# Kernel optimization log

Hardware: AMD Instinct MI355X
Metric: run time of the kernel (lower is better)

Reference implementation:

```python
import jax, jax.numpy as jnp
import numpy as np

B, S, D, H = 2, 2048, 1024, 16
HD = D // H  # head_dim = 64


def setup_inputs() -> dict:
    key = jax.random.key(0)
    ks = jax.random.split(key, 7)
    scale = 0.02
    return {
        "q": jax.random.normal(ks[0], (B, S, D), dtype=jnp.float32),
        "k": jax.random.normal(ks[1], (B, S, D), dtype=jnp.float32),
        "v": jax.random.normal(ks[2], (B, S, D), dtype=jnp.float32),
        "Wq": jax.random.normal(ks[3], (D, D), dtype=jnp.float32) * scale,
        "Wk": jax.random.normal(ks[4], (D, D), dtype=jnp.float32) * scale,
        "Wv": jax.random.normal(ks[5], (D, D), dtype=jnp.float32) * scale,
        "Wo": jax.random.normal(ks[6], (D, D), dtype=jnp.float32) * scale,
    }


def reference(q, k, v, Wq, Wk, Wv, Wo):
    # bias-free linear projections (torch Linear: y = x @ W.T)
    qh = (q @ Wq.T).reshape(B, S, H, HD).transpose(0, 2, 1, 3)  # b h t d
    kh = (k @ Wk.T).reshape(B, S, H, HD).transpose(0, 2, 1, 3)
    vh = (v @ Wv.T).reshape(B, S, H, HD).transpose(0, 2, 1, 3)

    scores = jnp.einsum("bhqd,bhkd->bhqk", qh, kh) / jnp.sqrt(jnp.float32(HD))
    # max_subtract: NOTE faithful to source - max taken BEFORE causal masking
    scores = scores - jnp.max(scores, axis=-1, keepdims=True)
    # causal mask (strict upper triangle -> -inf)
    causal_mask = jnp.triu(jnp.ones((S, S), dtype=bool), k=1)
    scores = jnp.where(causal_mask, -jnp.inf, scores)
    num = jnp.exp(scores)
    den = jnp.sum(num, axis=-1, keepdims=True) + 1.0  # quiet softmax (+1 denominator)
    attn = num / den

    out = jnp.einsum("bhqk,bhkd->bhqd", attn, vh)
    out = out.transpose(0, 2, 1, 3).reshape(B, S, D)  # b t (h d)
    return out @ Wo.T
```

## Files before the change

kernel.cpp:

```cpp
#include <hip/hip_runtime.h>
#include <hip/hip_bf16.h>

#define B_  2
#define S_  2048
#define D_  1024
#define H_  16
#define HD_ 64

typedef __attribute__((ext_vector_type(4))) short s16x4;
typedef __attribute__((ext_vector_type(8))) short s16x8;
typedef __attribute__((ext_vector_type(4))) float f32x4;
typedef __attribute__((ext_vector_type(8))) __bf16 bf16x8;

__device__ __forceinline__ unsigned short f2bf(float x) {
  union { float f; unsigned int u; } un; un.f = x;
  unsigned int r = un.u + 0x7fffu + ((un.u >> 16) & 1u);
  return (unsigned short)(r >> 16);
}

__device__ __forceinline__ f32x4 fz4() { f32x4 z = {0.f, 0.f, 0.f, 0.f}; return z; }

__device__ __forceinline__ f32x4 mfma32(s16x8 a, s16x8 b, f32x4 c) {
  return __builtin_amdgcn_mfma_f32_16x16x32_bf16(
      __builtin_bit_cast(bf16x8, a), __builtin_bit_cast(bf16x8, b), c, 0, 0, 0);
}

__device__ __forceinline__ void gload16(void* lds_base, const void* gsrc) {
  __builtin_amdgcn_global_load_lds(
      (const __attribute__((address_space(1))) unsigned int*)gsrc,
      (__attribute__((address_space(3))) unsigned int*)lds_base, 16, 0, 0);
}

__global__ __launch_bounds__(256) void cvt_all(const float4* __restrict__ q,
                                               const float4* __restrict__ k,
                                               const float4* __restrict__ v,
                                               const float4* __restrict__ wq,
                                               const float4* __restrict__ wk,
                                               const float4* __restrict__ wv,
                                               const float4* __restrict__ wo,
                                               uint2* __restrict__ oq, uint2* __restrict__ ok,
                                               uint2* __restrict__ ov, uint2* __restrict__ owq,
                                               uint2* __restrict__ owk, uint2* __restrict__ owv,
                                               uint2* __restrict__ owo) {
  int i = blockIdx.x * 256 + threadIdx.x;
  int st = gridDim.x * 256;
  for (; i < 4194304; i += st) {
    const float4* s; uint2* d; int off;
    if (i < 3145728) {
      int t = i >> 20; off = i & 1048575;
      s = (t == 0) ? q : (t == 1 ? k : v);
      d = (t == 0) ? oq : (t == 1 ? ok : ov);
    } else {
      int j = i - 3145728;
      int t = j >> 18; off = j & 262143;
      s = (t == 0) ? wq : (t == 1 ? wk : (t == 2 ? wv : wo));
      d = (t == 0) ? owq : (t == 1 ? owk : (t == 2 ? owv : owo));
    }
    float4 x = s[off];
    uint2 o;
    o.x = (unsigned)f2bf(x.x) | ((unsigned)f2bf(x.y) << 16);
    o.y = (unsigned)f2bf(x.z) | ((unsigned)f2bf(x.w) << 16);
    d[off] = o;
  }
}

template<int BM, int MODE, int NG>
__global__ __launch_bounds__(256) void gemm_bt(
    const unsigned short* __restrict__ A0, const unsigned short* __restrict__ A1,
    const unsigned short* __restrict__ A2,
    const unsigned short* __restrict__ W0, const unsigned short* __restrict__ W1,
    const unsigned short* __restrict__ W2,
    unsigned short* __restrict__ ob0, unsigned short* __restrict__ ob1,
    unsigned short* __restrict__ ob2, float* __restrict__ of) {
  __shared__ unsigned short As[2][BM * 32];
  __shared__ unsigned short Bs[2][128 * 32];
  const int tid  = threadIdx.x;
  const int lane = tid & 63;
  const int w    = tid >> 6;
  const int l15  = lane & 15, g = lane >> 4;

  int m0, n0;
  const unsigned short *A, *W;
  unsigned short* obf;
  float scale = 1.0f;
  if (NG == 3) {
    int swz = ((int)blockIdx.x & 7) * 96 + ((int)blockIdx.x >> 3);
    int p  = swz >> 5;
    int gi = p >> 3;
    n0 = (p & 7) * 128;
    m0 = (swz & 31) * 128;
    A   = gi == 0 ? A0 : (gi == 1 ? A1 : A2);
    W   = gi == 0 ? W0 : (gi == 1 ? W1 : W2);
    obf = gi == 0 ? ob0 : (gi == 1 ? ob1 : ob2);
    scale = (gi == 0) ? 0.125f : 1.0f;
  } else {
    int swz = ((int)blockIdx.x & 7) * 64 + ((int)blockIdx.x >> 3);
    m0 = (swz & 63) * BM;
    n0 = (swz >> 6) * 128;
    A = A0; W = W0; obf = ob0;
  }

  constexpr int MI  = (BM == 128) ? 4 : 2;
  const int wr = (w >> 1) * (MI * 16);
  const int wc = (w & 1) * 64;

  f32x4 acc[MI][4];
  #pragma unroll
  for (int i = 0; i < MI; i++)
    #pragma unroll
    for (int j = 0; j < 4; j++) acc[i][j] = fz4();

  const int srow = w * 16 + (lane >> 2);
  const int scol = ((lane & 3) ^ ((lane >> 2) & 3)) * 8;

  #define STAGE(buf, k0)                                                          \
    {                                                                             \
      _Pragma("unroll")                                                           \
      for (int i = 0; i < BM / 64; i++)                                           \
        gload16(&As[buf][(i * 64 + w * 16) * 32],                                 \
                &A[(size_t)(m0 + i * 64 + srow) * D_ + (k0) + scol]);             \
      _Pragma("unroll")                                                           \
      for (int i = 0; i < 2; i++)                                                 \
        gload16(&Bs[buf][(i * 64 + w * 16) * 32],                                 \
                &W[(size_t)(n0 + i * 64 + srow) * D_ + (k0) + scol]);             \
    }

  STAGE(0, 0);
  __syncthreads();
  int buf = 0;
  for (int t = 0; t < 32; ++t) {
    if (t < 31) STAGE(buf ^ 1, (t + 1) * 32);
    s16x8 af[MI], bfr[4];
    #pragma unroll
    for (int mi = 0; mi < MI; mi++)
      af[mi] = *(const s16x8*)&As[buf][(wr + mi * 16 + l15) * 32 + ((g ^ (l15 & 3)) * 8)];
    #pragma unroll
    for (int ni = 0; ni < 4; ni++)
      bfr[ni] = *(const s16x8*)&Bs[buf][(wc + ni * 16 + l15) * 32 + ((g ^ (l15 & 3)) * 8)];
    __builtin_amdgcn_s_setprio(1);
    #pragma unroll
    for (int mi = 0; mi < MI; mi++)
      #pragma unroll
      for (int ni = 0; ni < 4; ni++)
        acc[mi][ni] = mfma32(af[mi], bfr[ni], acc[mi][ni]);
    __builtin_amdgcn_s_setprio(0);
    __syncthreads();
    buf ^= 1;
  }
  #undef STAGE

  #pragma unroll
  for (int mi = 0; mi < MI; mi++)
    #pragma unroll
    for (int ni = 0; ni < 4; ni++)
      #pragma unroll
      for (int j = 0; j < 4; j++) {
        int r = m0 + wr + mi * 16 + 4 * g + j;
        int c = n0 + wc + ni * 16 + l15;
        float v = acc[mi][ni][j] * scale;
        if (MODE == 0) {
          int b = r >> 11, s = r & (S_ - 1), h = c >> 6, hd = c & 63;
          obf[(((size_t)(b * H_ + h)) * S_ + s) * HD_ + hd] = f2bf(v);
        } else {
          of[(size_t)r * D_ + c] = v;
        }
      }
}

__global__ __launch_bounds__(512) void attn_kernel(const unsigned short* __restrict__ Qh,
                                                   const unsigned short* __restrict__ Kh,
                                                   const unsigned short* __restrict__ Vh,
                                                   unsigned short* __restrict__ AO) {
  __shared__ unsigned short Ks[2][64 * 64];
  __shared__ unsigned short Vt[2][64 * 76];
  const int tid  = threadIdx.x;
  const int lane = tid & 63;
  const int w    = tid >> 6;
  const int wq   = w & 3;
  const int grp  = w >> 2;
  const int l15  = lane & 15, g = lane >> 4;

  int swz = ((int)blockIdx.x & 7) * 64 + ((int)blockIdx.x >> 3);
  const int bh = swz >> 4;
  const int pr = swz & 15;
  const int qtA = pr, qtB = 31 - pr;
  const int myqt  = grp ? qtB : qtA;
  const int qtMax = qtB;
  const int q0 = myqt * 64;
  const unsigned short* Qb = Qh + (size_t)bh * S_ * HD_;
  const unsigned short* Kb = Kh + (size_t)bh * S_ * HD_;
  const unsigned short* Vb = Vh + (size_t)bh * S_ * HD_;

  const int qrow = q0 + wq * 16 + l15;
  s16x8 qf[2];
  #pragma unroll
  for (int kk = 0; kk < 2; kk++)
    qf[kk] = *(const s16x8*)&Qb[(size_t)qrow * HD_ + kk * 32 + 8 * g];

  float m = -INFINITY, l = 0.f;
  f32x4 outa[4];
  #pragma unroll
  for (int d = 0; d < 4; d++) outa[d] = fz4();

  const int srow_l = lane >> 3;
  const int scol = ((lane & 7) ^ ((lane >> 3) & 7)) * 8;
  const int vkey = tid & 63;
  const int vhd0 = (tid >> 6) * 8;

  #define STAGE_K(kblk, b)                                                        \
    gload16(&Ks[b][(w * 8) * 64],                                                 \
            &Kb[(size_t)((kblk) * 64 + w * 8 + srow_l) * HD_ + scol]);
  #define LOAD_V(kblk, vr)                                                        \
    vr = *(const uint4*)&Vb[(size_t)((kblk) * 64 + vkey) * HD_ + vhd0];
  #define WRITE_V(b, vr)                                                          \
    {                                                                             \
      unsigned int u[4] = {vr.x, vr.y, vr.z, vr.w};                               \
      _Pragma("unroll")                                                           \
      for (int c2 = 0; c2 < 4; c2++) {                                            \
        Vt[b][(vhd0 + 2 * c2    ) * 76 + vkey] = (unsigned short)(u[c2] & 0xffffu); \
        Vt[b][(vhd0 + 2 * c2 + 1) * 76 + vkey] = (unsigned short)(u[c2] >> 16);   \
      }                                                                           \
    }

  {
    STAGE_K(0, 0);
    uint4 vr0;
    LOAD_V(0, vr0);
    WRITE_V(0, vr0);
    __syncthreads();
  }

  for (int t = 0; t < 32; ++t) {
    const int cur = t & 1, nxt = cur ^ 1;
    const int k0 = t * 64;
    if (t < 31) STAGE_K(t + 1, nxt);
    uint4 vr;
    const bool vnext = (t < 31) && (t + 1 <= qtMax);
    if (vnext) LOAD_V(t + 1, vr);

    f32x4 sf[4];
    #pragma unroll
    for (int kt = 0; kt < 4; kt++) sf[kt] = fz4();
    __builtin_amdgcn_s_setprio(1);
    #pragma unroll
    for (int kt = 0; kt < 4; kt++)
      #pragma unroll
      for (int kk = 0; kk < 2; kk++) {
        s16x8 kf = *(const s16x8*)&Ks[cur][(kt * 16 + l15) * 64 + (((kk * 4 + g) ^ (l15 & 7)) * 8)];
        sf[kt] = mfma32(kf, qf[kk], sf[kt]);
      }
    __builtin_amdgcn_s_setprio(0);

    float bm = -INFINITY;
    #pragma unroll
    for (int kt = 0; kt < 4; kt++)
      #pragma unroll
      for (int j = 0; j < 4; j++) bm = fmaxf(bm, sf[kt][j]);
    bm = fmaxf(bm, __shfl_xor(bm, 16));
    bm = fmaxf(bm, __shfl_xor(bm, 32));
    if (__any(bm > m)) {
      float mn  = fmaxf(m, bm);
      float fsc = __expf(m - mn);
      m = mn;
      l *= fsc;
      #pragma unroll
      for (int d = 0; d < 4; d++)
        #pragma unroll
        for (int j = 0; j < 4; j++) outa[d][j] *= fsc;
    }

    if (t <= myqt) {
      s16x8 pfs[2];
      float rs = 0.f;
      if (t == myqt) {
        #pragma unroll
        for (int kt2 = 0; kt2 < 2; kt2++)
          #pragma unroll
          for (int j = 0; j < 4; j++) {
            int keyg = k0 + kt2 * 32 + 4 * g + j;
            float e = (keyg <= qrow) ? __expf(sf[2 * kt2][j] - m) : 0.f;
            rs += e;
            pfs[kt2][j] = (short)f2bf(e);
            float e2 = (keyg + 16 <= qrow) ? __expf(sf[2 * kt2 + 1][j] - m) : 0.f;
            rs += e2;
            pfs[kt2][4 + j] = (short)f2bf(e2);
          }
      } else {
        #pragma unroll
        for (int kt2 = 0; kt2 < 2; kt2++)
          #pragma unroll
          for (int j = 0; j < 4; j++) {
            float e = __expf(sf[2 * kt2][j] - m);
            rs += e;
            pfs[kt2][j] = (short)f2bf(e);
            float e2 = __expf(sf[2 * kt2 + 1][j] - m);
            rs += e2;
            pfs[kt2][4 + j] = (short)f2bf(e2);
          }
      }
      rs += __shfl_xor(rs, 16);
      rs += __shfl_xor(rs, 32);
      l += rs;
      __builtin_amdgcn_s_setprio(1);
      #pragma unroll
      for (int d = 0; d < 4; d++)
        #pragma unroll
        for (int kt2 = 0; kt2 < 2; kt2++) {
          s16x4 vlo = *(const s16x4*)&Vt[cur][(d * 16 + l15) * 76 + kt2 * 32 + 4 * g];
          s16x4 vhi = *(const s16x4*)&Vt[cur][(d * 16 + l15) * 76 + kt2 * 32 + 16 + 4 * g];
          s16x8 vv = {vlo[0], vlo[1], vlo[2], vlo[3], vhi[0], vhi[1], vhi[2], vhi[3]};
          outa[d] = mfma32(vv, pfs[kt2], outa[d]);
        }
      __builtin_amdgcn_s_setprio(0);
    }

    if (vnext) WRITE_V(nxt, vr);
    __syncthreads();
  }
  #undef STAGE_K
  #undef LOAD_V
  #undef WRITE_V

  const float inv = 1.f / (l + 1.f);
  const int b = bh >> 4, h = bh & 15;
  #pragma unroll
  for (int d = 0; d < 4; d++) {
    uint2 o;
    o.x = (unsigned)f2bf(outa[d][0] * inv) | ((unsigned)f2bf(outa[d][1] * inv) << 16);
    o.y = (unsigned)f2bf(outa[d][2] * inv) | ((unsigned)f2bf(outa[d][3] * inv) << 16);
    *(uint2*)&AO[(size_t)(b * S_ + qrow) * D_ + h * 64 + d * 16 + 4 * g] = o;
  }
}

extern "C" void kernel_launch(void* const* d_in, const int* in_sizes, int n_in,
                              void* d_out, int out_size, void* d_ws, size_t ws_size,
                              hipStream_t stream) {
  const float* q  = (const float*)d_in[0];
  const float* k  = (const float*)d_in[1];
  const float* v  = (const float*)d_in[2];
  const float* Wq = (const float*)d_in[3];
  const float* Wk = (const float*)d_in[4];
  const float* Wv = (const float*)d_in[5];
  const float* Wo = (const float*)d_in[6];

  unsigned short* ws  = (unsigned short*)d_ws;
  unsigned short* qb  = ws;
  unsigned short* kb  = qb  + 4194304;
  unsigned short* vb  = kb  + 4194304;
  unsigned short* Wqb = vb  + 4194304;
  unsigned short* Wkb = Wqb + 1048576;
  unsigned short* Wvb = Wkb + 1048576;
  unsigned short* Wob = Wvb + 1048576;
  unsigned short* Qh  = Wob + 1048576;
  unsigned short* Kh  = Qh  + 4194304;
  unsigned short* Vh  = Kh  + 4194304;
  unsigned short* AO  = Vh  + 4194304;

  cvt_all<<<2048, 256, 0, stream>>>((const float4*)q, (const float4*)k, (const float4*)v,
                                    (const float4*)Wq, (const float4*)Wk, (const float4*)Wv,
                                    (const float4*)Wo,
                                    (uint2*)qb, (uint2*)kb, (uint2*)vb, (uint2*)Wqb,
                                    (uint2*)Wkb, (uint2*)Wvb, (uint2*)Wob);

  gemm_bt<128, 0, 3><<<768, 256, 0, stream>>>(qb, kb, vb, Wqb, Wkb, Wvb,
                                              Qh, Kh, Vh, nullptr);

  attn_kernel<<<512, 512, 0, stream>>>(Qh, Kh, Vh, AO);

  gemm_bt<64, 1, 1><<<512, 256, 0, stream>>>(AO, nullptr, nullptr, Wob, nullptr, nullptr,
                                             nullptr, nullptr, nullptr, (float*)d_out);
}
```

Baseline: 223.9 us.

## Replace QKV projection GEMM with 256x256-tile, 8-wave pipelined kernel

The fused QKV projection moves from 128x128 tiles with 4 waves and BK=32 to 256x256 tiles with 8 waves and BK=64. Each 256-row A slice and W slice is then loaded far fewer times, cutting global and LDS traffic per MFMA. Global loads for the next K tile are interleaved with MFMA quadrants using explicit vmcnt/lgkmcnt waits and barriers, with XOR-swizzled LDS addressing. The cost is 192 blocks on a GPU with many CUs, which may underfill the device, plus heavy register pressure from 128 accumulator vectors per thread. The output projection is split into its own specialised kernel with no functional change.

```diff
diff --git a/kernel.cpp b/kernel.cpp
--- a/kernel.cpp
+++ b/kernel.cpp
@@ -64,49 +64,145 @@
   }
 }
 
-template<int BM, int MODE, int NG>
-__global__ __launch_bounds__(256) void gemm_bt(
+__global__ __launch_bounds__(512, 2) void qkv256(
     const unsigned short* __restrict__ A0, const unsigned short* __restrict__ A1,
     const unsigned short* __restrict__ A2,
     const unsigned short* __restrict__ W0, const unsigned short* __restrict__ W1,
     const unsigned short* __restrict__ W2,
     unsigned short* __restrict__ ob0, unsigned short* __restrict__ ob1,
-    unsigned short* __restrict__ ob2, float* __restrict__ of) {
-  __shared__ unsigned short As[2][BM * 32];
+    unsigned short* __restrict__ ob2) {
+  __shared__ unsigned short As[2][16384];
+  __shared__ unsigned short Bs[2][16384];
+  const int tid  = threadIdx.x;
+  const int lane = tid & 63;
+  const int w    = tid >> 6;
+  const int l15  = lane & 15, g = lane >> 4;
+  const int wm   = w >> 2;
+  const int wn   = w & 3;
+
+  int swz = ((int)blockIdx.x & 7) * 24 + ((int)blockIdx.x >> 3);
+  const int nt = swz / 48;
+  const int mt = swz % 48;
+  const int gi = mt >> 4;
+  const int m0 = (mt & 15) * 256;
+  const int n0 = nt * 256;
+  const unsigned short* A = gi == 0 ? A0 : (gi == 1 ? A1 : A2);
+  const unsigned short* W = gi == 0 ? W0 : (gi == 1 ? W1 : W2);
+  unsigned short* obf     = gi == 0 ? ob0 : (gi == 1 ? ob1 : ob2);
+  const float scale = (gi == 0) ? 0.125f : 1.0f;
+
+  f32x4 acc[8][4];
+  #pragma unroll
+  for (int i = 0; i < 8; i++)
+    #pragma unroll
+    for (int j = 0; j < 4; j++) acc[i][j] = fz4();
+
+  const int srow_i = w * 8 + (lane >> 3);
+  const int scol   = ((lane & 7) ^ ((lane >> 3) & 7)) * 8;
+
+  #define SG_A(nb, i, kt) gload16(&As[nb][((i) * 512 + w * 64) * 8],                     \
+      &A[(size_t)(m0 + (i) * 64 + srow_i) * D_ + (kt) * 64 + scol])
+  #define SG_B(nb, i, kt) gload16(&Bs[nb][((i) * 512 + w * 64) * 8],                     \
+      &W[(size_t)(n0 + (i) * 64 + srow_i) * D_ + (kt) * 64 + scol])
+
+  #define RD_A(dst, mq, bufi)                                                            \
+    _Pragma("unroll") for (int fi = 0; fi < 4; fi++)                                     \
+      _Pragma("unroll") for (int kk = 0; kk < 2; kk++)                                   \
+        dst[fi][kk] = *(const s16x8*)&As[bufi][(wm * 128 + (mq) * 64 + fi * 16 + l15) * 64 \
+                                              + (((kk * 4 + g) ^ (l15 & 7)) * 8)];
+  #define RD_B(dst, nq, bufi)                                                            \
+    _Pragma("unroll") for (int fj = 0; fj < 2; fj++)                                     \
+      _Pragma("unroll") for (int kk = 0; kk < 2; kk++)                                   \
+        dst[fj][kk] = *(const s16x8*)&Bs[bufi][(wn * 64 + (nq) * 32 + fj * 16 + l15) * 64  \
+                                              + (((kk * 4 + g) ^ (l15 & 7)) * 8)];
+  #define MM(mq, nq, av, bv)                                                             \
+    _Pragma("unroll") for (int fi = 0; fi < 4; fi++)                                     \
+      _Pragma("unroll") for (int fj = 0; fj < 2; fj++)                                   \
+        _Pragma("unroll") for (int kk = 0; kk < 2; kk++)                                 \
+          acc[(mq) * 4 + fi][(nq) * 2 + fj] =                                            \
+              mfma32(av[fi][kk], bv[fj][kk], acc[(mq) * 4 + fi][(nq) * 2 + fj]);
+
+  SG_A(0, 0, 0); SG_A(0, 2, 0);
+  SG_B(0, 0, 0); SG_B(0, 1, 0); SG_B(0, 2, 0); SG_B(0, 3, 0);
+  SG_A(0, 1, 0); SG_A(0, 3, 0);
+
+  s16x8 a[4][2], b0[2][2], b1[2][2];
+  for (int t = 0; t < 16; ++t) {
+    const int buf = t & 1, nb = buf ^ 1;
+    const int tn = (t + 1) & 15;
+    asm volatile("s_waitcnt vmcnt(2)" ::: "memory");
+    __builtin_amdgcn_s_barrier();
+    RD_A(a, 0, buf);
+    RD_B(b0, 0, buf);
+    SG_A(nb, 0, tn); SG_A(nb, 2, tn);
+    asm volatile("s_waitcnt lgkmcnt(0)" ::: "memory");
+    __builtin_amdgcn_s_setprio(1);
+    MM(0, 0, a, b0);
+    __builtin_amdgcn_s_setprio(0);
+    __builtin_amdgcn_s_barrier();
+    RD_B(b1, 1, buf);
+    SG_B(nb, 0, tn); SG_B(nb, 1, tn); SG_B(nb, 2, tn); SG_B(nb, 3, tn);
+    asm volatile("s_waitcnt lgkmcnt(0)" ::: "memory");
+    __builtin_amdgcn_s_setprio(1);
+    MM(0, 1, a, b1);
+    __builtin_amdgcn_s_setprio(0);
+    __builtin_amdgcn_s_barrier();
+    asm volatile("s_waitcnt vmcnt(6)" ::: "memory");
+    __builtin_amdgcn_s_barrier();
+    RD_A(a, 1, buf);
+    SG_A(nb, 1, tn); SG_A(nb, 3, tn);
+    asm volatile("s_waitcnt lgkmcnt(0)" ::: "memory");
+    __builtin_amdgcn_s_setprio(1);
+    MM(1, 1, a, b1);
+    __builtin_amdgcn_s_setprio(0);
+    __builtin_amdgcn_s_barrier();
+    RD_B(b0, 0, buf);
+    asm volatile("s_waitcnt lgkmcnt(0)" ::: "memory");
+    __builtin_amdgcn_s_setprio(1);
+    MM(1, 0, a, b0);
+    __builtin_amdgcn_s_setprio(0);
+    __builtin_amdgcn_s_barrier();
+  }
+  asm volatile("s_waitcnt vmcnt(0)" ::: "memory");
+
+  #undef SG_A
+  #undef SG_B
+  #undef RD_A
+  #undef RD_B
+  #undef MM
+
+  #pragma unroll
+  for (int mi = 0; mi < 8; mi++)
+    #pragma unroll
+    for (int ni = 0; ni < 4; ni++)
+      #pragma unroll
+      for (int j = 0; j < 4; j++) {
+        int r = m0 + wm * 128 + mi * 16 + 4 * g + j;
+        int c = n0 + wn * 64 + ni * 16 + l15;
+        float v = acc[mi][ni][j] * scale;
+        int b = r >> 11, s = r & (S_ - 1), h = c >> 6, hd = c & 63;
+        obf[(((size_t)(b * H_ + h)) * S_ + s) * HD_ + hd] = f2bf(v);
+      }
+}
+
+__global__ __launch_bounds__(256) void gemm_wo(const unsigned short* __restrict__ A,
+                                               const unsigned short* __restrict__ W,
+                                               float* __restrict__ of) {
+  __shared__ unsigned short As[2][64 * 32];
   __shared__ unsigned short Bs[2][128 * 32];
   const int tid  = threadIdx.x;
   const int lane = tid & 63;
   const int w    = tid >> 6;
   const int l15  = lane & 15, g = lane >> 4;
 
-  int m0, n0;
-  const unsigned short *A, *W;
-  unsigned short* obf;
-  float scale = 1.0f;
-  if (NG == 3) {
-    int swz = ((int)blockIdx.x & 7) * 96 + ((int)blockIdx.x >> 3);
-    int p  = swz >> 5;
-    int gi = p >> 3;
-    n0 = (p & 7) * 128;
-    m0 = (swz & 31) * 128;
-    A   = gi == 0 ? A0 : (gi == 1 ? A1 : A2);
-    W   = gi == 0 ? W0 : (gi == 1 ? W1 : W2);
-    obf = gi == 0 ? ob0 : (gi == 1 ? ob1 : ob2);
-    scale = (gi == 0) ? 0.125f : 1.0f;
-  } else {
-    int swz = ((int)blockIdx.x & 7) * 64 + ((int)blockIdx.x >> 3);
-    m0 = (swz & 63) * BM;
-    n0 = (swz >> 6) * 128;
-    A = A0; W = W0; obf = ob0;
-  }
-
-  constexpr int MI  = (BM == 128) ? 4 : 2;
-  const int wr = (w >> 1) * (MI * 16);
-  const int wc = (w & 1) * 64;
-
-  f32x4 acc[MI][4];
-  #pragma unroll
-  for (int i = 0; i < MI; i++)
+  int swz = ((int)blockIdx.x & 7) * 64 + ((int)blockIdx.x >> 3);
+  const int m0 = (swz & 63) * 64;
+  const int n0 = (swz >> 6) * 128;
+  const int wr = (w >> 1) * 32, wc = (w & 1) * 64;
+
+  f32x4 acc[2][4];
+  #pragma unroll
+  for (int i = 0; i < 2; i++)
     #pragma unroll
     for (int j = 0; j < 4; j++) acc[i][j] = fz4();
 
@@ -115,10 +211,8 @@
 
   #define STAGE(buf, k0)                                                          \
     {                                                                             \
-      _Pragma("unroll")                                                           \
-      for (int i = 0; i < BM / 64; i++)                                           \
-        gload16(&As[buf][(i * 64 + w * 16) * 32],                                 \
-                &A[(size_t)(m0 + i * 64 + srow) * D_ + (k0) + scol]);             \
+      gload16(&As[buf][(w * 16) * 32],                                            \
+              &A[(size_t)(m0 + srow) * D_ + (k0) + scol]);                        \
       _Pragma("unroll")                                                           \
       for (int i = 0; i < 2; i++)                                                 \
         gload16(&Bs[buf][(i * 64 + w * 16) * 32],                                 \
@@ -130,16 +224,16 @@
   int buf = 0;
   for (int t = 0; t < 32; ++t) {
     if (t < 31) STAGE(buf ^ 1, (t + 1) * 32);
-    s16x8 af[MI], bfr[4];
-    #pragma unroll
-    for (int mi = 0; mi < MI; mi++)
+    s16x8 af[2], bfr[4];
+    #pragma unroll
+    for (int mi = 0; mi < 2; mi++)
       af[mi] = *(const s16x8*)&As[buf][(wr + mi * 16 + l15) * 32 + ((g ^ (l15 & 3)) * 8)];
     #pragma unroll
     for (int ni = 0; ni < 4; ni++)
       bfr[ni] = *(const s16x8*)&Bs[buf][(wc + ni * 16 + l15) * 32 + ((g ^ (l15 & 3)) * 8)];
     __builtin_amdgcn_s_setprio(1);
     #pragma unroll
-    for (int mi = 0; mi < MI; mi++)
+    for (int mi = 0; mi < 2; mi++)
       #pragma unroll
       for (int ni = 0; ni < 4; ni++)
         acc[mi][ni] = mfma32(af[mi], bfr[ni], acc[mi][ni]);
@@ -150,20 +244,14 @@
   #undef STAGE
 
   #pragma unroll
-  for (int mi = 0; mi < MI; mi++)
+  for (int mi = 0; mi < 2; mi++)
     #pragma unroll
     for (int ni = 0; ni < 4; ni++)
       #pragma unroll
       for (int j = 0; j < 4; j++) {
         int r = m0 + wr + mi * 16 + 4 * g + j;
         int c = n0 + wc + ni * 16 + l15;
-        float v = acc[mi][ni][j] * scale;
-        if (MODE == 0) {
-          int b = r >> 11, s = r & (S_ - 1), h = c >> 6, hd = c & 63;
-          obf[(((size_t)(b * H_ + h)) * S_ + s) * HD_ + hd] = f2bf(v);
-        } else {
-          of[(size_t)r * D_ + c] = v;
-        }
+        of[(size_t)r * D_ + c] = acc[mi][ni][j];
       }
 }
 
@@ -362,11 +450,9 @@
                                     (uint2*)qb, (uint2*)kb, (uint2*)vb, (uint2*)Wqb,
                                     (uint2*)Wkb, (uint2*)Wvb, (uint2*)Wob);
 
-  gemm_bt<128, 0, 3><<<768, 256, 0, stream>>>(qb, kb, vb, Wqb, Wkb, Wvb,
-                                              Qh, Kh, Vh, nullptr);
+  qkv256<<<192, 512, 0, stream>>>(qb, kb, vb, Wqb, Wkb, Wvb, Qh, Kh, Vh);
 
   attn_kernel<<<512, 512, 0, stream>>>(Qh, Kh, Vh, AO);
 
-  gemm_bt<64, 1, 1><<<512, 256, 0, stream>>>(AO, nullptr, nullptr, Wob, nullptr, nullptr,
-                                             nullptr, nullptr, nullptr, (float*)d_out);
-}
+  gemm_wo<<<512, 256, 0, stream>>>(AO, Wob, (float*)d_out);
+}
```

New measurement: 219.7 us. Within noise of the previous version (-1.9%).
